# Optimization experiments

Hardware: AMD Instinct MI355X
Metric: run time of the kernel (lower is better)

The kernel has to match this reference:

```python
import jax, jax.numpy as jnp
import numpy as np
from jax import lax

B, N, C_PTS = 16, 4096, 64
NPOINT, RADIUS, NSAMPLE = 1024, 0.2, 32
MLP = [64, 64, 128]


def setup_inputs() -> dict:
    key = jax.random.key(0)
    ks = jax.random.split(key, 8)
    inp = {
        "xyz": jax.random.uniform(ks[0], (B, N, 3), jnp.float32),
        "points": jax.random.normal(ks[1], (B, N, C_PTS), jnp.float32),
    }
    cin = C_PTS + 3  # use_xyz=True concatenates centered xyz
    for i, cout in enumerate(MLP):
        inp[f"W{i}"] = jax.random.normal(ks[2 + 2 * i], (cin, cout), jnp.float32) / np.sqrt(cin).astype(np.float32)
        inp[f"b{i}"] = jnp.zeros((cout,), jnp.float32)
        cin = cout
    return inp


def _fps(xyz, npoint):
    # Farthest point sampling (sequential) -> (B, npoint) int32 indices.
    b, n, _ = xyz.shape

    def body(carry, _):
        mind, far = carry  # mind: (B,N) running min sq-dist, far: (B,) current pick
        cen = jnp.take_along_axis(xyz, far[:, None, None], axis=1)  # (B,1,3)
        d = jnp.sum((xyz - cen) ** 2, -1)  # (B,N)
        mind = jnp.minimum(mind, d)
        nxt = jnp.argmax(mind, -1).astype(jnp.int32)
        return (mind, nxt), far

    init = (jnp.full((b, n), 1e10, jnp.float32), jnp.zeros((b,), jnp.int32))
    _, idx = lax.scan(body, init, None, length=npoint)
    return jnp.transpose(idx)  # (B, npoint)


def _ball_query(radius, nsample, xyz, new_xyz):
    # First `nsample` point indices (in original order) within `radius` of each
    # center; short groups padded with the first found index (TF op semantics).
    n = xyz.shape[1]
    d2 = jnp.sum((new_xyz[:, :, None, :] - xyz[:, None, :, :]) ** 2, -1)  # (B,S,N)
    keyv = jnp.where(d2 <= radius * radius, jnp.arange(n, dtype=jnp.int32), n)
    idx = jnp.sort(keyv, axis=-1)[:, :, :nsample]  # smallest indices first
    first = idx[:, :, :1]
    idx = jnp.where(idx == n, first, idx)
    return jnp.minimum(idx, n - 1)


def _group(t, idx):
    # t: (B,N,C), idx: (B,S,K) -> (B,S,K,C)
    return jax.vmap(lambda tb, ib: tb[ib])(t, idx)


def reference(xyz, points, W0, b0, W1, b1, W2, b2):
    fps_idx = _fps(xyz, NPOINT)  # (B,S)
    new_xyz = jnp.take_along_axis(xyz, fps_idx[..., None], axis=1)  # (B,S,3)
    idx = _ball_query(RADIUS, NSAMPLE, xyz, new_xyz)  # (B,S,K)
    grouped_xyz = _group(xyz, idx) - new_xyz[:, :, None, :]  # (B,S,K,3) centered
    grouped_pts = _group(points, idx)  # (B,S,K,C)
    new_points = jnp.concatenate([grouped_xyz, grouped_pts], -1)  # (B,S,K,3+C)
    for W, b in ((W0, b0), (W1, b1), (W2, b2)):  # shared MLP = 1x1 conv + relu
        new_points = jax.nn.relu(jnp.einsum('bskc,cd->bskd', new_points, W) + b)
    new_points = jnp.max(new_points, axis=2)  # max-pool over neighbors -> (B,S,128)
    return new_xyz, new_points, idx
```

## Files before the change

### kernel.cpp

```cpp
#include <hip/hip_runtime.h>

#define NB      16
#define NPTS    4096
#define NPOINT  1024
#define NSAMPLE 32

typedef float v2f __attribute__((ext_vector_type(2)));

__device__ __forceinline__ v2f pk_add(v2f a, v2f b) {
  v2f d;
  asm("v_pk_add_f32 %0, %1, %2" : "=v"(d) : "v"(a), "v"(b));
  return d;
}
__device__ __forceinline__ v2f pk_mul(v2f a, v2f b) {
  v2f d;
  asm("v_pk_mul_f32 %0, %1, %2" : "=v"(d) : "v"(a), "v"(b));
  return d;
}
__device__ __forceinline__ float fnegx(float x) {
  return __int_as_float(__float_as_int(x) ^ 0x80000000);
}

template <int C>
__device__ __forceinline__ int dppi(int v) {
  return __builtin_amdgcn_update_dpp(0, v, C, 0xf, 0xf, true);
}

template <int C>
__device__ __forceinline__ unsigned long long dppmax_u64(unsigned long long k) {
  int lo = dppi<C>((int)(unsigned)k);
  int hi = dppi<C>((int)(k >> 32));
  unsigned long long o = ((unsigned long long)(unsigned)hi << 32) | (unsigned)lo;
  return o > k ? o : k;
}

__device__ __forceinline__ unsigned long long swzmax16_u64(unsigned long long k) {
  int lo = __builtin_amdgcn_ds_swizzle((int)(unsigned)k, 0x401F);
  int hi = __builtin_amdgcn_ds_swizzle((int)(k >> 32), 0x401F);
  unsigned long long o = ((unsigned long long)(unsigned)hi << 32) | (unsigned)lo;
  return o > k ? o : k;
}

__global__ __launch_bounds__(512) void fps_kernel(const float* __restrict__ xyz,
                                                  float* __restrict__ out_xyz) {
  __shared__ float lx[NPTS], ly[NPTS], lz[NPTS];
  __shared__ float scen[NPOINT * 3];
  __shared__ unsigned long long part[2][16];
  const int b = blockIdx.x, t = threadIdx.x;
  const int lane = t & 63;
  const int wid = t >> 6;
  const float* g = xyz + (size_t)b * NPTS * 3;
  for (int j = t; j < NPTS; j += 512) {
    lx[j] = g[3 * j]; ly[j] = g[3 * j + 1]; lz[j] = g[3 * j + 2];
  }
  __syncthreads();
  v2f px2[4], py2[4], pz2[4], mind2[4];
  unsigned nlo[8];
#pragma unroll
  for (int p = 0; p < 4; ++p) {
    const int j0 = t + 512 * (2 * p);
    px2[p] = (v2f){lx[j0], lx[j0 + 512]};
    py2[p] = (v2f){ly[j0], ly[j0 + 512]};
    pz2[p] = (v2f){lz[j0], lz[j0 + 512]};
    mind2[p] = (v2f){1e10f, 1e10f};
    nlo[2 * p] = ~(unsigned)j0;
    nlo[2 * p + 1] = ~(unsigned)(j0 + 512);
  }
  float cx = lx[0], cy = ly[0], cz = lz[0];
  for (int it = 0; it < NPOINT; ++it) {
    if (t == 0) {
      scen[3 * it] = cx; scen[3 * it + 1] = cy; scen[3 * it + 2] = cz;
    }
    const float ncx = fnegx(cx), ncy = fnegx(cy), ncz = fnegx(cz);
    const v2f ncxx = (v2f){ncx, ncx};
    const v2f ncyy = (v2f){ncy, ncy};
    const v2f nczz = (v2f){ncz, ncz};
#pragma unroll
    for (int p = 0; p < 4; ++p) {
      const v2f dx = pk_add(px2[p], ncxx);
      const v2f dy = pk_add(py2[p], ncyy);
      const v2f dz = pk_add(pz2[p], nczz);
      const v2f xx = pk_mul(dx, dx);
      const v2f yy = pk_mul(dy, dy);
      const v2f zz = pk_mul(dz, dz);
      v2f s = pk_add(xx, yy);
      s = pk_add(s, zz);
      mind2[p].x = fminf(mind2[p].x, s.x);
      mind2[p].y = fminf(mind2[p].y, s.y);
    }
    unsigned long long k[8];
#pragma unroll
    for (int p = 0; p < 4; ++p) {
      k[2 * p] = ((unsigned long long)__float_as_uint(mind2[p].x) << 32) | nlo[2 * p];
      k[2 * p + 1] =
          ((unsigned long long)__float_as_uint(mind2[p].y) << 32) | nlo[2 * p + 1];
    }
#pragma unroll
    for (int s = 4; s; s >>= 1)
#pragma unroll
      for (int i = 0; i < s; ++i) k[i] = k[i] > k[i + s] ? k[i] : k[i + s];
    unsigned long long key = k[0];
    key = dppmax_u64<0xB1>(key);
    key = dppmax_u64<0x4E>(key);
    key = dppmax_u64<0x141>(key);
    key = dppmax_u64<0x140>(key);
    key = swzmax16_u64(key);
    const int buf = it & 1;
    if ((lane & 31) == 0) part[buf][wid * 2 + (lane >> 5)] = key;
    __syncthreads();
    unsigned long long rk = part[buf][lane & 15];
    rk = dppmax_u64<0xB1>(rk);
    rk = dppmax_u64<0x4E>(rk);
    rk = dppmax_u64<0x141>(rk);
    rk = dppmax_u64<0x140>(rk);
    const unsigned idx = ~(unsigned)rk;
    cx = lx[idx]; cy = ly[idx]; cz = lz[idx];
  }
  __syncthreads();
  float* ob = out_xyz + (size_t)b * NPOINT * 3;
  for (int i = t; i < NPOINT * 3; i += 512) ob[i] = scen[i];
}

__global__ __launch_bounds__(256) void ballq_kernel(const float* __restrict__ xyz,
                                                    const float* __restrict__ new_xyz,
                                                    int* __restrict__ ballidx,
                                                    float* __restrict__ out_idx) {
  __shared__ int sidx[4][NSAMPLE];
  const int wv = threadIdx.x >> 6, lane = threadIdx.x & 63;
  const int q = blockIdx.x * 4 + wv;
  const int b = q >> 10;
  const float* g = xyz + (size_t)b * NPTS * 3;
  const float nx = new_xyz[(size_t)q * 3];
  const float ny = new_xyz[(size_t)q * 3 + 1];
  const float nz = new_xyz[(size_t)q * 3 + 2];
  const float r2 = (float)(0.2 * 0.2);
  int cnt = 0;
  for (int base = 0; base < NPTS; base += 64) {
    const int j = base + lane;
    const float dx = __fsub_rn(g[3 * j], nx);
    const float dy = __fsub_rn(g[3 * j + 1], ny);
    const float dz = __fsub_rn(g[3 * j + 2], nz);
    const float d2 = __fadd_rn(__fadd_rn(__fmul_rn(dx, dx), __fmul_rn(dy, dy)),
                               __fmul_rn(dz, dz));
    const bool hit = d2 <= r2;
    const unsigned long long m = __ballot(hit);
    const int pos = cnt + __popcll(m & ((1ull << lane) - 1ull));
    if (hit && pos < NSAMPLE) sidx[wv][pos] = j;
    cnt += __popcll(m);
    if (cnt >= NSAMPLE) break;
  }
  __syncthreads();
  const int capped = cnt < NSAMPLE ? cnt : NSAMPLE;
  if (lane < NSAMPLE) {
    const int v = sidx[wv][lane < capped ? lane : 0];
    ballidx[(size_t)q * NSAMPLE + lane] = v;
    out_idx[(size_t)q * NSAMPLE + lane] = (float)v;
  }
}

__global__ __launch_bounds__(256) void p1_kernel(const float* __restrict__ pts,
                                                 const float* __restrict__ W0,
                                                 float* __restrict__ P1) {
  __shared__ float sw[4096];
  const int t = threadIdx.x;
  {
    const float4* w4 = (const float4*)(W0 + 192);
    float4* s4 = (float4*)sw;
#pragma unroll
    for (int m = 0; m < 4; ++m) s4[t + 256 * m] = w4[t + 256 * m];
  }
  __syncthreads();
  const size_t r = (size_t)blockIdx.x * 256 + t;
  const float* prow = pts + r * 64;
  float acc[64];
#pragma unroll
  for (int d = 0; d < 64; ++d) acc[d] = 0.0f;
#pragma unroll
  for (int cq = 0; cq < 16; ++cq) {
    const float4 p4 = *(const float4*)(prow + cq * 4);
    const float pv[4] = {p4.x, p4.y, p4.z, p4.w};
#pragma unroll
    for (int u = 0; u < 4; ++u) {
      const int c = cq * 4 + u;
#pragma unroll
      for (int d4 = 0; d4 < 16; ++d4) {
        const float4 w = *(const float4*)(&sw[c * 64 + d4 * 4]);
        acc[d4 * 4 + 0] = fmaf(pv[u], w.x, acc[d4 * 4 + 0]);
        acc[d4 * 4 + 1] = fmaf(pv[u], w.y, acc[d4 * 4 + 1]);
        acc[d4 * 4 + 2] = fmaf(pv[u], w.z, acc[d4 * 4 + 2]);
        acc[d4 * 4 + 3] = fmaf(pv[u], w.w, acc[d4 * 4 + 3]);
      }
    }
  }
  float* o = P1 + r * 64;
#pragma unroll
  for (int d4 = 0; d4 < 16; ++d4)
    *(float4*)(o + d4 * 4) =
        make_float4(acc[d4 * 4], acc[d4 * 4 + 1], acc[d4 * 4 + 2], acc[d4 * 4 + 3]);
}

__global__ __launch_bounds__(256) void mlp_kernel(
    const float* __restrict__ xyz, const float* __restrict__ new_xyz,
    const int* __restrict__ ballidx, const float* __restrict__ P1,
    const float* __restrict__ W0, const float* __restrict__ b0,
    const float* __restrict__ W1, const float* __restrict__ b1,
    const float* __restrict__ W2, const float* __restrict__ b2,
    float* __restrict__ out_np) {
  const int t = threadIdx.x;
  const int item = blockIdx.x * 256 + t;
  const int k = item & 31;
  const int q = item >> 5;
  const int b = q >> 10;
  const int idx = ballidx[(size_t)q * 32 + k];
  const float nx = new_xyz[(size_t)q * 3];
  const float ny = new_xyz[(size_t)q * 3 + 1];
  const float nz = new_xyz[(size_t)q * 3 + 2];
  const float* p = xyz + ((size_t)b * NPTS + idx) * 3;
  const float dx = p[0] - nx, dy = p[1] - ny, dz = p[2] - nz;

  float h1[64];
  const float* p1r = P1 + ((size_t)b * NPTS + idx) * 64;
#pragma unroll
  for (int d4 = 0; d4 < 16; ++d4) {
    const float4 pv = *(const float4*)(p1r + d4 * 4);
    const float pe[4] = {pv.x, pv.y, pv.z, pv.w};
#pragma unroll
    for (int u = 0; u < 4; ++u) {
      const int d = d4 * 4 + u;
      const float v = pe[u] + dx * W0[d] + dy * W0[64 + d] + dz * W0[128 + d] + b0[d];
      h1[d] = fmaxf(v, 0.0f);
    }
  }

  float h2[64];
#pragma unroll
  for (int j4 = 0; j4 < 16; ++j4) {
    const float4 bb = *(const float4*)(&b1[j4 * 4]);
    h2[j4 * 4 + 0] = bb.x; h2[j4 * 4 + 1] = bb.y;
    h2[j4 * 4 + 2] = bb.z; h2[j4 * 4 + 3] = bb.w;
  }
#pragma unroll
  for (int c = 0; c < 64; ++c) {
    const float hc = h1[c];
#pragma unroll
    for (int j4 = 0; j4 < 16; ++j4) {
      const float4 w = *(const float4*)(&W1[c * 64 + j4 * 4]);
      h2[j4 * 4 + 0] = fmaf(hc, w.x, h2[j4 * 4 + 0]);
      h2[j4 * 4 + 1] = fmaf(hc, w.y, h2[j4 * 4 + 1]);
      h2[j4 * 4 + 2] = fmaf(hc, w.z, h2[j4 * 4 + 2]);
      h2[j4 * 4 + 3] = fmaf(hc, w.w, h2[j4 * 4 + 3]);
    }
  }
#pragma unroll
  for (int j = 0; j < 64; ++j) h2[j] = fmaxf(h2[j], 0.0f);

  float* outq = out_np + (size_t)q * 128;
  for (int jb = 0; jb < 4; ++jb) {
    float acc[32];
#pragma unroll
    for (int j8 = 0; j8 < 8; ++j8) {
      const float4 bb = *(const float4*)(&b2[jb * 32 + j8 * 4]);
      acc[j8 * 4 + 0] = bb.x; acc[j8 * 4 + 1] = bb.y;
      acc[j8 * 4 + 2] = bb.z; acc[j8 * 4 + 3] = bb.w;
    }
#pragma unroll
    for (int c = 0; c < 64; ++c) {
      const float hc = h2[c];
#pragma unroll
      for (int j8 = 0; j8 < 8; ++j8) {
        const float4 w = *(const float4*)(&W2[c * 128 + jb * 32 + j8 * 4]);
        acc[j8 * 4 + 0] = fmaf(hc, w.x, acc[j8 * 4 + 0]);
        acc[j8 * 4 + 1] = fmaf(hc, w.y, acc[j8 * 4 + 1]);
        acc[j8 * 4 + 2] = fmaf(hc, w.z, acc[j8 * 4 + 2]);
        acc[j8 * 4 + 3] = fmaf(hc, w.w, acc[j8 * 4 + 3]);
      }
    }
#pragma unroll
    for (int j = 0; j < 32; ++j) acc[j] = fmaxf(acc[j], 0.0f);
#pragma unroll
    for (int msk = 16; msk >= 1; msk >>= 1) {
#pragma unroll
      for (int j = 0; j < 32; ++j) acc[j] = fmaxf(acc[j], __shfl_xor(acc[j], msk, 64));
    }
    if (k == 0) {
#pragma unroll
      for (int j8 = 0; j8 < 8; ++j8)
        *(float4*)(outq + jb * 32 + j8 * 4) =
            make_float4(acc[j8 * 4 + 0], acc[j8 * 4 + 1], acc[j8 * 4 + 2], acc[j8 * 4 + 3]);
    }
  }
}

extern "C" void kernel_launch(void* const* d_in, const int* in_sizes, int n_in,
                              void* d_out, int out_size, void* d_ws, size_t ws_size,
                              hipStream_t stream) {
  const float* xyz = (const float*)d_in[0];
  const float* pts = (const float*)d_in[1];
  const float* W0  = (const float*)d_in[2];
  const float* b0  = (const float*)d_in[3];
  const float* W1  = (const float*)d_in[4];
  const float* b1  = (const float*)d_in[5];
  const float* W2  = (const float*)d_in[6];
  const float* b2  = (const float*)d_in[7];

  float* out      = (float*)d_out;
  float* out_xyz  = out;
  float* out_np   = out + 16 * 1024 * 3;
  float* out_idx  = out_np + 16 * 1024 * 128;

  int*   ballidx = (int*)d_ws;
  float* P1      = (float*)((char*)d_ws + (2u << 20));

  fps_kernel<<<NB, 512, 0, stream>>>(xyz, out_xyz);
  p1_kernel<<<256, 256, 0, stream>>>(pts, W0, P1);
  ballq_kernel<<<4096, 256, 0, stream>>>(xyz, out_xyz, ballidx, out_idx);
  mlp_kernel<<<2048, 256, 0, stream>>>(xyz, out_xyz, ballidx, P1,
                                       W0, b0, W1, b1, W2, b2, out_np);
}
```

Measured before the change: 953.4 us.

## Fuse FPS with P1 precompute and ball query with MLP into two kernels

Merges the FPS and P1 (points·W0) kernels into one launch, where the first 16 blocks run FPS and the rest compute P1, so P1 can overlap the sequential FPS. Ball query is fused into the MLP kernel, keeping neighbor indices in shared memory instead of writing them to a global workspace and reading them back. FPS point storage changes from three float arrays to float4 so each centroid fetch is a single LDS load. The cost is larger shared memory per FPS block and a ball-query phase inside each MLP block that runs before its MLP work.

```diff
diff --git a/kernel.cpp b/kernel.cpp
--- a/kernel.cpp
+++ b/kernel.cpp
@@ -41,177 +41,187 @@
   return o > k ? o : k;
 }
 
-__global__ __launch_bounds__(512) void fps_kernel(const float* __restrict__ xyz,
-                                                  float* __restrict__ out_xyz) {
-  __shared__ float lx[NPTS], ly[NPTS], lz[NPTS];
-  __shared__ float scen[NPOINT * 3];
-  __shared__ unsigned long long part[2][16];
-  const int b = blockIdx.x, t = threadIdx.x;
-  const int lane = t & 63;
-  const int wid = t >> 6;
-  const float* g = xyz + (size_t)b * NPTS * 3;
-  for (int j = t; j < NPTS; j += 512) {
-    lx[j] = g[3 * j]; ly[j] = g[3 * j + 1]; lz[j] = g[3 * j + 2];
-  }
-  __syncthreads();
-  v2f px2[4], py2[4], pz2[4], mind2[4];
-  unsigned nlo[8];
-#pragma unroll
-  for (int p = 0; p < 4; ++p) {
-    const int j0 = t + 512 * (2 * p);
-    px2[p] = (v2f){lx[j0], lx[j0 + 512]};
-    py2[p] = (v2f){ly[j0], ly[j0 + 512]};
-    pz2[p] = (v2f){lz[j0], lz[j0 + 512]};
-    mind2[p] = (v2f){1e10f, 1e10f};
-    nlo[2 * p] = ~(unsigned)j0;
-    nlo[2 * p + 1] = ~(unsigned)(j0 + 512);
-  }
-  float cx = lx[0], cy = ly[0], cz = lz[0];
-  for (int it = 0; it < NPOINT; ++it) {
-    if (t == 0) {
-      scen[3 * it] = cx; scen[3 * it + 1] = cy; scen[3 * it + 2] = cz;
-    }
-    const float ncx = fnegx(cx), ncy = fnegx(cy), ncz = fnegx(cz);
-    const v2f ncxx = (v2f){ncx, ncx};
-    const v2f ncyy = (v2f){ncy, ncy};
-    const v2f nczz = (v2f){ncz, ncz};
+union SharedA {
+  struct {
+    float4 lc4[NPTS];
+    float scen[NPOINT * 3];
+    unsigned long long part[2][16];
+  } f;
+  float sw[4096];
+};
+
+__global__ __launch_bounds__(512) void fps_p1_kernel(
+    const float* __restrict__ xyz, const float* __restrict__ pts,
+    const float* __restrict__ W0, float* __restrict__ out_xyz,
+    float* __restrict__ P1) {
+  __shared__ SharedA sm;
+  const int t = threadIdx.x;
+  if (blockIdx.x < NB) {
+    const int b = blockIdx.x;
+    const int lane = t & 63;
+    const int wid = t >> 6;
+    const float* g = xyz + (size_t)b * NPTS * 3;
+    for (int j = t; j < NPTS; j += 512)
+      sm.f.lc4[j] = make_float4(g[3 * j], g[3 * j + 1], g[3 * j + 2], 0.0f);
+    __syncthreads();
+    v2f px2[4], py2[4], pz2[4], mind2[4];
+    unsigned nlo[8];
 #pragma unroll
     for (int p = 0; p < 4; ++p) {
-      const v2f dx = pk_add(px2[p], ncxx);
-      const v2f dy = pk_add(py2[p], ncyy);
-      const v2f dz = pk_add(pz2[p], nczz);
-      const v2f xx = pk_mul(dx, dx);
-      const v2f yy = pk_mul(dy, dy);
-      const v2f zz = pk_mul(dz, dz);
-      v2f s = pk_add(xx, yy);
-      s = pk_add(s, zz);
-      mind2[p].x = fminf(mind2[p].x, s.x);
-      mind2[p].y = fminf(mind2[p].y, s.y);
-    }
-    unsigned long long k[8];
-#pragma unroll
-    for (int p = 0; p < 4; ++p) {
-      k[2 * p] = ((unsigned long long)__float_as_uint(mind2[p].x) << 32) | nlo[2 * p];
-      k[2 * p + 1] =
-          ((unsigned long long)__float_as_uint(mind2[p].y) << 32) | nlo[2 * p + 1];
-    }
-#pragma unroll
-    for (int s = 4; s; s >>= 1)
-#pragma unroll
-      for (int i = 0; i < s; ++i) k[i] = k[i] > k[i + s] ? k[i] : k[i + s];
-    unsigned long long key = k[0];
-    key = dppmax_u64<0xB1>(key);
-    key = dppmax_u64<0x4E>(key);
-    key = dppmax_u64<0x141>(key);
-    key = dppmax_u64<0x140>(key);
-    key = swzmax16_u64(key);
-    const int buf = it & 1;
-    if ((lane & 31) == 0) part[buf][wid * 2 + (lane >> 5)] = key;
+      const int j0 = t + 512 * (2 * p);
+      const float4 a = sm.f.lc4[j0];
+      const float4 c = sm.f.lc4[j0 + 512];
+      px2[p] = (v2f){a.x, c.x};
+      py2[p] = (v2f){a.y, c.y};
+      pz2[p] = (v2f){a.z, c.z};
+      mind2[p] = (v2f){1e10f, 1e10f};
+      nlo[2 * p] = ~(unsigned)j0;
+      nlo[2 * p + 1] = ~(unsigned)(j0 + 512);
+    }
+    float cx, cy, cz;
+    {
+      const float4 c0 = sm.f.lc4[0];
+      cx = c0.x; cy = c0.y; cz = c0.z;
+    }
+    for (int it = 0; it < NPOINT; ++it) {
+      if (t == 0) {
+        sm.f.scen[3 * it] = cx; sm.f.scen[3 * it + 1] = cy; sm.f.scen[3 * it + 2] = cz;
+      }
+      const float ncx = fnegx(cx), ncy = fnegx(cy), ncz = fnegx(cz);
+      const v2f ncxx = (v2f){ncx, ncx};
+      const v2f ncyy = (v2f){ncy, ncy};
+      const v2f nczz = (v2f){ncz, ncz};
+#pragma unroll
+      for (int p = 0; p < 4; ++p) {
+        const v2f dx = pk_add(px2[p], ncxx);
+        const v2f dy = pk_add(py2[p], ncyy);
+        const v2f dz = pk_add(pz2[p], nczz);
+        const v2f xx = pk_mul(dx, dx);
+        const v2f yy = pk_mul(dy, dy);
+        const v2f zz = pk_mul(dz, dz);
+        v2f s = pk_add(xx, yy);
+        s = pk_add(s, zz);
+        mind2[p].x = fminf(mind2[p].x, s.x);
+        mind2[p].y = fminf(mind2[p].y, s.y);
+      }
+      unsigned long long k[8];
+#pragma unroll
+      for (int p = 0; p < 4; ++p) {
+        k[2 * p] = ((unsigned long long)__float_as_uint(mind2[p].x) << 32) | nlo[2 * p];
+        k[2 * p + 1] =
+            ((unsigned long long)__float_as_uint(mind2[p].y) << 32) | nlo[2 * p + 1];
+      }
+#pragma unroll
+      for (int s = 4; s; s >>= 1)
+#pragma unroll
+        for (int i = 0; i < s; ++i) k[i] = k[i] > k[i + s] ? k[i] : k[i + s];
+      unsigned long long key = k[0];
+      key = dppmax_u64<0xB1>(key);
+      key = dppmax_u64<0x4E>(key);
+      key = dppmax_u64<0x141>(key);
+      key = dppmax_u64<0x140>(key);
+      key = swzmax16_u64(key);
+      const int buf = it & 1;
+      if ((lane & 31) == 0) sm.f.part[buf][wid * 2 + (lane >> 5)] = key;
+      __syncthreads();
+      unsigned long long rk = sm.f.part[buf][lane & 15];
+      rk = dppmax_u64<0xB1>(rk);
+      rk = dppmax_u64<0x4E>(rk);
+      rk = dppmax_u64<0x141>(rk);
+      rk = dppmax_u64<0x140>(rk);
+      const unsigned idx = ~(unsigned)rk;
+      const float4 c4 = sm.f.lc4[idx];
+      cx = c4.x; cy = c4.y; cz = c4.z;
+    }
     __syncthreads();
-    unsigned long long rk = part[buf][lane & 15];
-    rk = dppmax_u64<0xB1>(rk);
-    rk = dppmax_u64<0x4E>(rk);
-    rk = dppmax_u64<0x141>(rk);
-    rk = dppmax_u64<0x140>(rk);
-    const unsigned idx = ~(unsigned)rk;
-    cx = lx[idx]; cy = ly[idx]; cz = lz[idx];
-  }
-  __syncthreads();
-  float* ob = out_xyz + (size_t)b * NPOINT * 3;
-  for (int i = t; i < NPOINT * 3; i += 512) ob[i] = scen[i];
-}
-
-__global__ __launch_bounds__(256) void ballq_kernel(const float* __restrict__ xyz,
-                                                    const float* __restrict__ new_xyz,
-                                                    int* __restrict__ ballidx,
-                                                    float* __restrict__ out_idx) {
-  __shared__ int sidx[4][NSAMPLE];
-  const int wv = threadIdx.x >> 6, lane = threadIdx.x & 63;
-  const int q = blockIdx.x * 4 + wv;
-  const int b = q >> 10;
-  const float* g = xyz + (size_t)b * NPTS * 3;
-  const float nx = new_xyz[(size_t)q * 3];
-  const float ny = new_xyz[(size_t)q * 3 + 1];
-  const float nz = new_xyz[(size_t)q * 3 + 2];
-  const float r2 = (float)(0.2 * 0.2);
-  int cnt = 0;
-  for (int base = 0; base < NPTS; base += 64) {
-    const int j = base + lane;
-    const float dx = __fsub_rn(g[3 * j], nx);
-    const float dy = __fsub_rn(g[3 * j + 1], ny);
-    const float dz = __fsub_rn(g[3 * j + 2], nz);
-    const float d2 = __fadd_rn(__fadd_rn(__fmul_rn(dx, dx), __fmul_rn(dy, dy)),
-                               __fmul_rn(dz, dz));
-    const bool hit = d2 <= r2;
-    const unsigned long long m = __ballot(hit);
-    const int pos = cnt + __popcll(m & ((1ull << lane) - 1ull));
-    if (hit && pos < NSAMPLE) sidx[wv][pos] = j;
-    cnt += __popcll(m);
-    if (cnt >= NSAMPLE) break;
-  }
-  __syncthreads();
-  const int capped = cnt < NSAMPLE ? cnt : NSAMPLE;
-  if (lane < NSAMPLE) {
-    const int v = sidx[wv][lane < capped ? lane : 0];
-    ballidx[(size_t)q * NSAMPLE + lane] = v;
-    out_idx[(size_t)q * NSAMPLE + lane] = (float)v;
-  }
-}
-
-__global__ __launch_bounds__(256) void p1_kernel(const float* __restrict__ pts,
-                                                 const float* __restrict__ W0,
-                                                 float* __restrict__ P1) {
-  __shared__ float sw[4096];
-  const int t = threadIdx.x;
-  {
-    const float4* w4 = (const float4*)(W0 + 192);
-    float4* s4 = (float4*)sw;
-#pragma unroll
-    for (int m = 0; m < 4; ++m) s4[t + 256 * m] = w4[t + 256 * m];
-  }
-  __syncthreads();
-  const size_t r = (size_t)blockIdx.x * 256 + t;
-  const float* prow = pts + r * 64;
-  float acc[64];
-#pragma unroll
-  for (int d = 0; d < 64; ++d) acc[d] = 0.0f;
-#pragma unroll
-  for (int cq = 0; cq < 16; ++cq) {
-    const float4 p4 = *(const float4*)(prow + cq * 4);
-    const float pv[4] = {p4.x, p4.y, p4.z, p4.w};
-#pragma unroll
-    for (int u = 0; u < 4; ++u) {
-      const int c = cq * 4 + u;
-#pragma unroll
-      for (int d4 = 0; d4 < 16; ++d4) {
-        const float4 w = *(const float4*)(&sw[c * 64 + d4 * 4]);
-        acc[d4 * 4 + 0] = fmaf(pv[u], w.x, acc[d4 * 4 + 0]);
-        acc[d4 * 4 + 1] = fmaf(pv[u], w.y, acc[d4 * 4 + 1]);
-        acc[d4 * 4 + 2] = fmaf(pv[u], w.z, acc[d4 * 4 + 2]);
-        acc[d4 * 4 + 3] = fmaf(pv[u], w.w, acc[d4 * 4 + 3]);
-      }
-    }
-  }
-  float* o = P1 + r * 64;
-#pragma unroll
-  for (int d4 = 0; d4 < 16; ++d4)
-    *(float4*)(o + d4 * 4) =
-        make_float4(acc[d4 * 4], acc[d4 * 4 + 1], acc[d4 * 4 + 2], acc[d4 * 4 + 3]);
-}
-
-__global__ __launch_bounds__(256) void mlp_kernel(
+    float* ob = out_xyz + (size_t)b * NPOINT * 3;
+    for (int i = t; i < NPOINT * 3; i += 512) ob[i] = sm.f.scen[i];
+  } else {
+    {
+      const float4* w4 = (const float4*)(W0 + 192);
+      float4* s4 = (float4*)sm.sw;
+#pragma unroll
+      for (int m = 0; m < 2; ++m) s4[t + 512 * m] = w4[t + 512 * m];
+    }
+    __syncthreads();
+    const size_t r = (size_t)(blockIdx.x - NB) * 512 + t;
+    const float* prow = pts + r * 64;
+    float acc[64];
+#pragma unroll
+    for (int d = 0; d < 64; ++d) acc[d] = 0.0f;
+#pragma unroll
+    for (int cq = 0; cq < 16; ++cq) {
+      const float4 p4 = *(const float4*)(prow + cq * 4);
+      const float pv[4] = {p4.x, p4.y, p4.z, p4.w};
+#pragma unroll
+      for (int u = 0; u < 4; ++u) {
+        const int c = cq * 4 + u;
+#pragma unroll
+        for (int d4 = 0; d4 < 16; ++d4) {
+          const float4 w = *(const float4*)(&sm.sw[c * 64 + d4 * 4]);
+          acc[d4 * 4 + 0] = fmaf(pv[u], w.x, acc[d4 * 4 + 0]);
+          acc[d4 * 4 + 1] = fmaf(pv[u], w.y, acc[d4 * 4 + 1]);
+          acc[d4 * 4 + 2] = fmaf(pv[u], w.z, acc[d4 * 4 + 2]);
+          acc[d4 * 4 + 3] = fmaf(pv[u], w.w, acc[d4 * 4 + 3]);
+        }
+      }
+    }
+    float* o = P1 + r * 64;
+#pragma unroll
+    for (int d4 = 0; d4 < 16; ++d4)
+      *(float4*)(o + d4 * 4) =
+          make_float4(acc[d4 * 4], acc[d4 * 4 + 1], acc[d4 * 4 + 2], acc[d4 * 4 + 3]);
+  }
+}
+
+__global__ __launch_bounds__(256) void ballq_mlp_kernel(
     const float* __restrict__ xyz, const float* __restrict__ new_xyz,
-    const int* __restrict__ ballidx, const float* __restrict__ P1,
+    const float* __restrict__ P1,
     const float* __restrict__ W0, const float* __restrict__ b0,
     const float* __restrict__ W1, const float* __restrict__ b1,
     const float* __restrict__ W2, const float* __restrict__ b2,
-    float* __restrict__ out_np) {
+    float* __restrict__ out_np, float* __restrict__ out_idx) {
+  __shared__ int sidx[8][NSAMPLE];
   const int t = threadIdx.x;
-  const int item = blockIdx.x * 256 + t;
-  const int k = item & 31;
-  const int q = item >> 5;
+  const int wv = t >> 6, lane = t & 63;
+  const int qbase = blockIdx.x * 8;
+  const float r2 = (float)(0.2 * 0.2);
+  for (int s = 0; s < 2; ++s) {
+    const int ql = wv * 2 + s;
+    const int q = qbase + ql;
+    const int b = q >> 10;
+    const float* g = xyz + (size_t)b * NPTS * 3;
+    const float nx = new_xyz[(size_t)q * 3];
+    const float ny = new_xyz[(size_t)q * 3 + 1];
+    const float nz = new_xyz[(size_t)q * 3 + 2];
+    int cnt = 0;
+    for (int base = 0; base < NPTS; base += 64) {
+      const int j = base + lane;
+      const float dx = __fsub_rn(g[3 * j], nx);
+      const float dy = __fsub_rn(g[3 * j + 1], ny);
+      const float dz = __fsub_rn(g[3 * j + 2], nz);
+      const float d2 = __fadd_rn(__fadd_rn(__fmul_rn(dx, dx), __fmul_rn(dy, dy)),
+                                 __fmul_rn(dz, dz));
+      const bool hit = d2 <= r2;
+      const unsigned long long m = __ballot(hit);
+      const int pos = cnt + __popcll(m & ((1ull << lane) - 1ull));
+      if (hit && pos < NSAMPLE) sidx[ql][pos] = j;
+      cnt += __popcll(m);
+      if (cnt >= NSAMPLE) break;
+    }
+    const int capped = cnt < NSAMPLE ? cnt : NSAMPLE;
+    if (lane < NSAMPLE) {
+      const int v = sidx[ql][lane < capped ? lane : 0];
+      sidx[ql][lane] = v;
+      out_idx[(size_t)q * NSAMPLE + lane] = (float)v;
+    }
+  }
+  __syncthreads();
+  const int k = t & 31;
+  const int ql = t >> 5;
+  const int q = qbase + ql;
   const int b = q >> 10;
-  const int idx = ballidx[(size_t)q * 32 + k];
+  const int idx = sidx[ql][k];
   const float nx = new_xyz[(size_t)q * 3];
   const float ny = new_xyz[(size_t)q * 3 + 1];
   const float nz = new_xyz[(size_t)q * 3 + 2];
@@ -308,12 +318,10 @@
   float* out_np   = out + 16 * 1024 * 3;
   float* out_idx  = out_np + 16 * 1024 * 128;
 
-  int*   ballidx = (int*)d_ws;
-  float* P1      = (float*)((char*)d_ws + (2u << 20));
-
-  fps_kernel<<<NB, 512, 0, stream>>>(xyz, out_xyz);
-  p1_kernel<<<256, 256, 0, stream>>>(pts, W0, P1);
-  ballq_kernel<<<4096, 256, 0, stream>>>(xyz, out_xyz, ballidx, out_idx);
-  mlp_kernel<<<2048, 256, 0, stream>>>(xyz, out_xyz, ballidx, P1,
-                                       W0, b0, W1, b1, W2, b2, out_np);
-}
+  float* P1 = (float*)d_ws;
+
+  fps_p1_kernel<<<NB + 128, 512, 0, stream>>>(xyz, pts, W0, out_xyz, P1);
+  ballq_mlp_kernel<<<2048, 256, 0, stream>>>(xyz, out_xyz, P1,
+                                             W0, b0, W1, b1, W2, b2,
+                                             out_np, out_idx);
+}
```

Measured after the change: 1.006 ms. 5.5% more time.

## Merge FPS and P1 projection into one launch; use packed FMA in MLP

Applied to the files above, without the earlier changes.

Merges the sequential farthest-point-sampling kernel and the point-feature projection kernel into one launch. The first 16 blocks run FPS and the remaining 128 blocks compute P1, so the projection can run on otherwise idle CUs alongside the long serial FPS loop. Shared memory is unioned so both roles fit one kernel, though the padding gives every block about 84KB of LDS. The MLP layers 2 and 3 are also rewritten to use v_pk_fma_f32 on float pairs, halving FMA instruction count at the cost of possible register pressure and packing moves.

```diff
diff --git a/kernel.cpp b/kernel.cpp
--- a/kernel.cpp
+++ b/kernel.cpp
@@ -17,6 +17,11 @@
   asm("v_pk_mul_f32 %0, %1, %2" : "=v"(d) : "v"(a), "v"(b));
   return d;
 }
+__device__ __forceinline__ v2f pk_fma(v2f a, v2f b, v2f c) {
+  v2f d;
+  asm("v_pk_fma_f32 %0, %1, %2, %3" : "=v"(d) : "v"(a), "v"(b), "v"(c));
+  return d;
+}
 __device__ __forceinline__ float fnegx(float x) {
   return __int_as_float(__float_as_int(x) ^ 0x80000000);
 }
@@ -25,7 +30,6 @@
 __device__ __forceinline__ int dppi(int v) {
   return __builtin_amdgcn_update_dpp(0, v, C, 0xf, 0xf, true);
 }
-
 template <int C>
 __device__ __forceinline__ unsigned long long dppmax_u64(unsigned long long k) {
   int lo = dppi<C>((int)(unsigned)k);
@@ -33,7 +37,6 @@
   unsigned long long o = ((unsigned long long)(unsigned)hi << 32) | (unsigned)lo;
   return o > k ? o : k;
 }
-
 __device__ __forceinline__ unsigned long long swzmax16_u64(unsigned long long k) {
   int lo = __builtin_amdgcn_ds_swizzle((int)(unsigned)k, 0x401F);
   int hi = __builtin_amdgcn_ds_swizzle((int)(k >> 32), 0x401F);
@@ -41,84 +44,130 @@
   return o > k ? o : k;
 }
 
-__global__ __launch_bounds__(512) void fps_kernel(const float* __restrict__ xyz,
-                                                  float* __restrict__ out_xyz) {
-  __shared__ float lx[NPTS], ly[NPTS], lz[NPTS];
-  __shared__ float scen[NPOINT * 3];
-  __shared__ unsigned long long part[2][16];
-  const int b = blockIdx.x, t = threadIdx.x;
-  const int lane = t & 63;
-  const int wid = t >> 6;
-  const float* g = xyz + (size_t)b * NPTS * 3;
-  for (int j = t; j < NPTS; j += 512) {
-    lx[j] = g[3 * j]; ly[j] = g[3 * j + 1]; lz[j] = g[3 * j + 2];
-  }
-  __syncthreads();
-  v2f px2[4], py2[4], pz2[4], mind2[4];
-  unsigned nlo[8];
-#pragma unroll
-  for (int p = 0; p < 4; ++p) {
-    const int j0 = t + 512 * (2 * p);
-    px2[p] = (v2f){lx[j0], lx[j0 + 512]};
-    py2[p] = (v2f){ly[j0], ly[j0 + 512]};
-    pz2[p] = (v2f){lz[j0], lz[j0 + 512]};
-    mind2[p] = (v2f){1e10f, 1e10f};
-    nlo[2 * p] = ~(unsigned)j0;
-    nlo[2 * p + 1] = ~(unsigned)(j0 + 512);
-  }
-  float cx = lx[0], cy = ly[0], cz = lz[0];
-  for (int it = 0; it < NPOINT; ++it) {
-    if (t == 0) {
-      scen[3 * it] = cx; scen[3 * it + 1] = cy; scen[3 * it + 2] = cz;
-    }
-    const float ncx = fnegx(cx), ncy = fnegx(cy), ncz = fnegx(cz);
-    const v2f ncxx = (v2f){ncx, ncx};
-    const v2f ncyy = (v2f){ncy, ncy};
-    const v2f nczz = (v2f){ncz, ncz};
+union SharedB {
+  struct {
+    float lx[NPTS], ly[NPTS], lz[NPTS];
+    float scen[NPOINT * 3];
+    unsigned long long part[2][16];
+  } f;
+  float sw[4096];
+  char pad[86016];
+};
+
+__global__ __launch_bounds__(512) void fps_p1_kernel(
+    const float* __restrict__ xyz, const float* __restrict__ pts,
+    const float* __restrict__ W0, float* __restrict__ out_xyz,
+    float* __restrict__ P1) {
+  __shared__ SharedB sm;
+  const int t = threadIdx.x;
+  if (blockIdx.x < NB) {
+    const int b = blockIdx.x;
+    const int lane = t & 63;
+    const float* g = xyz + (size_t)b * NPTS * 3;
+    for (int j = t; j < NPTS; j += 512) {
+      sm.f.lx[j] = g[3 * j]; sm.f.ly[j] = g[3 * j + 1]; sm.f.lz[j] = g[3 * j + 2];
+    }
+    __syncthreads();
+    v2f px2[4], py2[4], pz2[4], mind2[4];
+    unsigned nlo[8];
 #pragma unroll
     for (int p = 0; p < 4; ++p) {
-      const v2f dx = pk_add(px2[p], ncxx);
-      const v2f dy = pk_add(py2[p], ncyy);
-      const v2f dz = pk_add(pz2[p], nczz);
-      const v2f xx = pk_mul(dx, dx);
-      const v2f yy = pk_mul(dy, dy);
-      const v2f zz = pk_mul(dz, dz);
-      v2f s = pk_add(xx, yy);
-      s = pk_add(s, zz);
-      mind2[p].x = fminf(mind2[p].x, s.x);
-      mind2[p].y = fminf(mind2[p].y, s.y);
-    }
-    unsigned long long k[8];
-#pragma unroll
-    for (int p = 0; p < 4; ++p) {
-      k[2 * p] = ((unsigned long long)__float_as_uint(mind2[p].x) << 32) | nlo[2 * p];
-      k[2 * p + 1] =
-          ((unsigned long long)__float_as_uint(mind2[p].y) << 32) | nlo[2 * p + 1];
-    }
-#pragma unroll
-    for (int s = 4; s; s >>= 1)
-#pragma unroll
-      for (int i = 0; i < s; ++i) k[i] = k[i] > k[i + s] ? k[i] : k[i + s];
-    unsigned long long key = k[0];
-    key = dppmax_u64<0xB1>(key);
-    key = dppmax_u64<0x4E>(key);
-    key = dppmax_u64<0x141>(key);
-    key = dppmax_u64<0x140>(key);
-    key = swzmax16_u64(key);
-    const int buf = it & 1;
-    if ((lane & 31) == 0) part[buf][wid * 2 + (lane >> 5)] = key;
+      const int j0 = t + 512 * (2 * p);
+      px2[p] = (v2f){sm.f.lx[j0], sm.f.lx[j0 + 512]};
+      py2[p] = (v2f){sm.f.ly[j0], sm.f.ly[j0 + 512]};
+      pz2[p] = (v2f){sm.f.lz[j0], sm.f.lz[j0 + 512]};
+      mind2[p] = (v2f){1e10f, 1e10f};
+      nlo[2 * p] = ~(unsigned)j0;
+      nlo[2 * p + 1] = ~(unsigned)(j0 + 512);
+    }
+    float cx = sm.f.lx[0], cy = sm.f.ly[0], cz = sm.f.lz[0];
+    for (int it = 0; it < NPOINT; ++it) {
+      if (t == 0) {
+        sm.f.scen[3 * it] = cx; sm.f.scen[3 * it + 1] = cy; sm.f.scen[3 * it + 2] = cz;
+      }
+      const float ncx = fnegx(cx), ncy = fnegx(cy), ncz = fnegx(cz);
+      const v2f ncxx = (v2f){ncx, ncx};
+      const v2f ncyy = (v2f){ncy, ncy};
+      const v2f nczz = (v2f){ncz, ncz};
+#pragma unroll
+      for (int p = 0; p < 4; ++p) {
+        const v2f dx = pk_add(px2[p], ncxx);
+        const v2f dy = pk_add(py2[p], ncyy);
+        const v2f dz = pk_add(pz2[p], nczz);
+        const v2f xx = pk_mul(dx, dx);
+        const v2f yy = pk_mul(dy, dy);
+        const v2f zz = pk_mul(dz, dz);
+        v2f s = pk_add(xx, yy);
+        s = pk_add(s, zz);
+        mind2[p].x = fminf(mind2[p].x, s.x);
+        mind2[p].y = fminf(mind2[p].y, s.y);
+      }
+      unsigned long long k[8];
+#pragma unroll
+      for (int p = 0; p < 4; ++p) {
+        k[2 * p] = ((unsigned long long)__float_as_uint(mind2[p].x) << 32) | nlo[2 * p];
+        k[2 * p + 1] =
+            ((unsigned long long)__float_as_uint(mind2[p].y) << 32) | nlo[2 * p + 1];
+      }
+#pragma unroll
+      for (int s = 4; s; s >>= 1)
+#pragma unroll
+        for (int i = 0; i < s; ++i) k[i] = k[i] > k[i + s] ? k[i] : k[i + s];
+      unsigned long long key = k[0];
+      key = dppmax_u64<0xB1>(key);
+      key = dppmax_u64<0x4E>(key);
+      key = dppmax_u64<0x141>(key);
+      key = dppmax_u64<0x140>(key);
+      key = swzmax16_u64(key);
+      const int buf = it & 1;
+      if ((lane & 31) == 0) sm.f.part[buf][(t >> 6) * 2 + (lane >> 5)] = key;
+      __syncthreads();
+      unsigned long long rk = sm.f.part[buf][lane & 15];
+      rk = dppmax_u64<0xB1>(rk);
+      rk = dppmax_u64<0x4E>(rk);
+      rk = dppmax_u64<0x141>(rk);
+      rk = dppmax_u64<0x140>(rk);
+      const unsigned idx = ~(unsigned)rk;
+      cx = sm.f.lx[idx]; cy = sm.f.ly[idx]; cz = sm.f.lz[idx];
+    }
     __syncthreads();
-    unsigned long long rk = part[buf][lane & 15];
-    rk = dppmax_u64<0xB1>(rk);
-    rk = dppmax_u64<0x4E>(rk);
-    rk = dppmax_u64<0x141>(rk);
-    rk = dppmax_u64<0x140>(rk);
-    const unsigned idx = ~(unsigned)rk;
-    cx = lx[idx]; cy = ly[idx]; cz = lz[idx];
-  }
-  __syncthreads();
-  float* ob = out_xyz + (size_t)b * NPOINT * 3;
-  for (int i = t; i < NPOINT * 3; i += 512) ob[i] = scen[i];
+    float* ob = out_xyz + (size_t)b * NPOINT * 3;
+    for (int i = t; i < NPOINT * 3; i += 512) ob[i] = sm.f.scen[i];
+  } else {
+    {
+      const float4* w4 = (const float4*)(W0 + 192);
+      float4* s4 = (float4*)sm.sw;
+      s4[t] = w4[t]; s4[t + 512] = w4[t + 512];
+    }
+    __syncthreads();
+    const size_t r = (size_t)(blockIdx.x - NB) * 512 + t;
+    const float* prow = pts + r * 64;
+    float acc[64];
+#pragma unroll
+    for (int d = 0; d < 64; ++d) acc[d] = 0.0f;
+#pragma unroll
+    for (int cq = 0; cq < 16; ++cq) {
+      const float4 p4 = *(const float4*)(prow + cq * 4);
+      const float pv[4] = {p4.x, p4.y, p4.z, p4.w};
+#pragma unroll
+      for (int u = 0; u < 4; ++u) {
+        const int c = cq * 4 + u;
+#pragma unroll
+        for (int d4 = 0; d4 < 16; ++d4) {
+          const float4 w = *(const float4*)(&sm.sw[c * 64 + d4 * 4]);
+          acc[d4 * 4 + 0] = fmaf(pv[u], w.x, acc[d4 * 4 + 0]);
+          acc[d4 * 4 + 1] = fmaf(pv[u], w.y, acc[d4 * 4 + 1]);
+          acc[d4 * 4 + 2] = fmaf(pv[u], w.z, acc[d4 * 4 + 2]);
+          acc[d4 * 4 + 3] = fmaf(pv[u], w.w, acc[d4 * 4 + 3]);
+        }
+      }
+    }
+    float* o = P1 + r * 64;
+#pragma unroll
+    for (int d4 = 0; d4 < 16; ++d4)
+      *(float4*)(o + d4 * 4) = make_float4(acc[d4 * 4 + 0], acc[d4 * 4 + 1],
+                                           acc[d4 * 4 + 2], acc[d4 * 4 + 3]);
+  }
 }
 
 __global__ __launch_bounds__(256) void ballq_kernel(const float* __restrict__ xyz,
@@ -158,47 +207,6 @@
   }
 }
 
-__global__ __launch_bounds__(256) void p1_kernel(const float* __restrict__ pts,
-                                                 const float* __restrict__ W0,
-                                                 float* __restrict__ P1) {
-  __shared__ float sw[4096];
-  const int t = threadIdx.x;
-  {
-    const float4* w4 = (const float4*)(W0 + 192);
-    float4* s4 = (float4*)sw;
-#pragma unroll
-    for (int m = 0; m < 4; ++m) s4[t + 256 * m] = w4[t + 256 * m];
-  }
-  __syncthreads();
-  const size_t r = (size_t)blockIdx.x * 256 + t;
-  const float* prow = pts + r * 64;
-  float acc[64];
-#pragma unroll
-  for (int d = 0; d < 64; ++d) acc[d] = 0.0f;
-#pragma unroll
-  for (int cq = 0; cq < 16; ++cq) {
-    const float4 p4 = *(const float4*)(prow + cq * 4);
-    const float pv[4] = {p4.x, p4.y, p4.z, p4.w};
-#pragma unroll
-    for (int u = 0; u < 4; ++u) {
-      const int c = cq * 4 + u;
-#pragma unroll
-      for (int d4 = 0; d4 < 16; ++d4) {
-        const float4 w = *(const float4*)(&sw[c * 64 + d4 * 4]);
-        acc[d4 * 4 + 0] = fmaf(pv[u], w.x, acc[d4 * 4 + 0]);
-        acc[d4 * 4 + 1] = fmaf(pv[u], w.y, acc[d4 * 4 + 1]);
-        acc[d4 * 4 + 2] = fmaf(pv[u], w.z, acc[d4 * 4 + 2]);
-        acc[d4 * 4 + 3] = fmaf(pv[u], w.w, acc[d4 * 4 + 3]);
-      }
-    }
-  }
-  float* o = P1 + r * 64;
-#pragma unroll
-  for (int d4 = 0; d4 < 16; ++d4)
-    *(float4*)(o + d4 * 4) =
-        make_float4(acc[d4 * 4], acc[d4 * 4 + 1], acc[d4 * 4 + 2], acc[d4 * 4 + 3]);
-}
-
 __global__ __launch_bounds__(256) void mlp_kernel(
     const float* __restrict__ xyz, const float* __restrict__ new_xyz,
     const int* __restrict__ ballidx, const float* __restrict__ P1,
@@ -232,51 +240,55 @@
     }
   }
 
-  float h2[64];
+  v2f h2p[32];
 #pragma unroll
   for (int j4 = 0; j4 < 16; ++j4) {
     const float4 bb = *(const float4*)(&b1[j4 * 4]);
-    h2[j4 * 4 + 0] = bb.x; h2[j4 * 4 + 1] = bb.y;
-    h2[j4 * 4 + 2] = bb.z; h2[j4 * 4 + 3] = bb.w;
+    h2p[2 * j4] = (v2f){bb.x, bb.y};
+    h2p[2 * j4 + 1] = (v2f){bb.z, bb.w};
   }
 #pragma unroll
   for (int c = 0; c < 64; ++c) {
-    const float hc = h1[c];
+    const v2f hc2 = (v2f){h1[c], h1[c]};
 #pragma unroll
     for (int j4 = 0; j4 < 16; ++j4) {
       const float4 w = *(const float4*)(&W1[c * 64 + j4 * 4]);
-      h2[j4 * 4 + 0] = fmaf(hc, w.x, h2[j4 * 4 + 0]);
-      h2[j4 * 4 + 1] = fmaf(hc, w.y, h2[j4 * 4 + 1]);
-      h2[j4 * 4 + 2] = fmaf(hc, w.z, h2[j4 * 4 + 2]);
-      h2[j4 * 4 + 3] = fmaf(hc, w.w, h2[j4 * 4 + 3]);
-    }
-  }
-#pragma unroll
-  for (int j = 0; j < 64; ++j) h2[j] = fmaxf(h2[j], 0.0f);
+      h2p[2 * j4] = pk_fma(hc2, (v2f){w.x, w.y}, h2p[2 * j4]);
+      h2p[2 * j4 + 1] = pk_fma(hc2, (v2f){w.z, w.w}, h2p[2 * j4 + 1]);
+    }
+  }
+#pragma unroll
+  for (int j = 0; j < 32; ++j) {
+    h2p[j].x = fmaxf(h2p[j].x, 0.0f);
+    h2p[j].y = fmaxf(h2p[j].y, 0.0f);
+  }
 
   float* outq = out_np + (size_t)q * 128;
   for (int jb = 0; jb < 4; ++jb) {
-    float acc[32];
+    v2f accp[16];
 #pragma unroll
     for (int j8 = 0; j8 < 8; ++j8) {
       const float4 bb = *(const float4*)(&b2[jb * 32 + j8 * 4]);
-      acc[j8 * 4 + 0] = bb.x; acc[j8 * 4 + 1] = bb.y;
-      acc[j8 * 4 + 2] = bb.z; acc[j8 * 4 + 3] = bb.w;
+      accp[2 * j8] = (v2f){bb.x, bb.y};
+      accp[2 * j8 + 1] = (v2f){bb.z, bb.w};
     }
 #pragma unroll
     for (int c = 0; c < 64; ++c) {
-      const float hc = h2[c];
+      const float hcs = (c & 1) ? h2p[c >> 1].y : h2p[c >> 1].x;
+      const v2f hc2 = (v2f){hcs, hcs};
 #pragma unroll
       for (int j8 = 0; j8 < 8; ++j8) {
         const float4 w = *(const float4*)(&W2[c * 128 + jb * 32 + j8 * 4]);
-        acc[j8 * 4 + 0] = fmaf(hc, w.x, acc[j8 * 4 + 0]);
-        acc[j8 * 4 + 1] = fmaf(hc, w.y, acc[j8 * 4 + 1]);
-        acc[j8 * 4 + 2] = fmaf(hc, w.z, acc[j8 * 4 + 2]);
-        acc[j8 * 4 + 3] = fmaf(hc, w.w, acc[j8 * 4 + 3]);
-      }
-    }
-#pragma unroll
-    for (int j = 0; j < 32; ++j) acc[j] = fmaxf(acc[j], 0.0f);
+        accp[2 * j8] = pk_fma(hc2, (v2f){w.x, w.y}, accp[2 * j8]);
+        accp[2 * j8 + 1] = pk_fma(hc2, (v2f){w.z, w.w}, accp[2 * j8 + 1]);
+      }
+    }
+    float acc[32];
+#pragma unroll
+    for (int j = 0; j < 16; ++j) {
+      acc[2 * j] = fmaxf(accp[j].x, 0.0f);
+      acc[2 * j + 1] = fmaxf(accp[j].y, 0.0f);
+    }
 #pragma unroll
     for (int msk = 16; msk >= 1; msk >>= 1) {
 #pragma unroll
@@ -284,9 +296,11 @@
     }
     if (k == 0) {
 #pragma unroll
-      for (int j8 = 0; j8 < 8; ++j8)
+      for (int j8 = 0; j8 < 8; ++j8) {
         *(float4*)(outq + jb * 32 + j8 * 4) =
-            make_float4(acc[j8 * 4 + 0], acc[j8 * 4 + 1], acc[j8 * 4 + 2], acc[j8 * 4 + 3]);
+            make_float4(acc[4 * j8 + 0], acc[4 * j8 + 1],
+                        acc[4 * j8 + 2], acc[4 * j8 + 3]);
+      }
     }
   }
 }
@@ -311,8 +325,7 @@
   int*   ballidx = (int*)d_ws;
   float* P1      = (float*)((char*)d_ws + (2u << 20));
 
-  fps_kernel<<<NB, 512, 0, stream>>>(xyz, out_xyz);
-  p1_kernel<<<256, 256, 0, stream>>>(pts, W0, P1);
+  fps_p1_kernel<<<NB + 128, 512, 0, stream>>>(xyz, pts, W0, out_xyz, P1);
   ballq_kernel<<<4096, 256, 0, stream>>>(xyz, out_xyz, ballidx, out_idx);
   mlp_kernel<<<2048, 256, 0, stream>>>(xyz, out_xyz, ballidx, P1,
                                        W0, b0, W1, b1, W2, b2, out_np);
```

After: 1.204 ms. 26.3% more time.
